# Performance work log

Measured on AMD Instinct MI355X. Metric: run time of the kernel, lower is better.

## Reference

```python
import jax, jax.numpy as jnp
import numpy as np

B, N, D, C = 8, 400, 768, 3
K = 0.4
# Original keeps ranked positions whose argsort value (original index) < k*N.
# That count is static: M = #{j in [0,N) : j < k*N}
M = int(np.sum(np.arange(N) < K * N))  # 160
# static off-diagonal pair index lists (i != j), row-major like the nested loops
_ii, _jj = np.nonzero(~np.eye(M, dtype=bool))
II = jnp.asarray(_ii)
JJ = jnp.asarray(_jj)


def setup_inputs() -> dict:
    key = jax.random.key(0)
    k1, k2, k3, k4 = jax.random.split(key, 4)
    x = jax.random.normal(k1, (B, N, D), dtype=jnp.float32)
    w_span = jax.random.normal(k2, (D, 1), dtype=jnp.float32) * 0.02
    b_span = jnp.zeros((1,), dtype=jnp.float32)
    w_pair = jax.random.normal(k3, (3 * D, C), dtype=jnp.float32) * 0.02
    b_pair = jnp.zeros((C,), dtype=jnp.float32)
    span_ranges = jax.random.randint(k4, (N, 2), 0, 40, dtype=jnp.int32)
    return {"x": x, "w_span": w_span, "b_span": b_span,
            "w_pair": w_pair, "b_pair": b_pair, "span_ranges": span_ranges}


def reference(x, w_span, b_span, w_pair, b_pair, span_ranges):
    # span scorer: Linear(D,1) + sigmoid -> [B, N]
    h = jax.nn.sigmoid(x @ w_span + b_span)[..., 0]
    # torch.argsort(descending=True)
    order = jnp.argsort(-h, axis=-1)  # [B, N], original span indices in rank order
    # keep ranked positions j where order[b, j] < k*N (exactly M per row)
    pos = jnp.sort(jnp.where(order < K * N, jnp.arange(N), N), axis=-1)[:, :M]  # [B, M]
    # gather selected spans (built under no_grad in the original)
    x_ranked = jax.lax.stop_gradient(jnp.take_along_axis(x, pos[:, :, None], axis=1))  # [B, M, D]
    ranges_ranked = span_ranges[pos]  # [B, M, 2]

    # pair scorer decomposed over the concat [x_i, x_j, x_i*x_j]
    w1, w2, w3 = w_pair[:D], w_pair[D:2 * D], w_pair[2 * D:]
    a = x_ranked @ w1  # [B, M, C] contribution of x_i
    b = x_ranked @ w2  # [B, M, C] contribution of x_j
    mult = x_ranked[:, :, None, :] * x_ranked[:, None, :, :]  # [B, M, M, D]
    logits = a[:, :, None, :] + b[:, None, :, :] + mult @ w3 + b_pair  # [B, M, M, C]
    probs = jax.nn.softmax(jax.nn.sigmoid(logits), axis=-1)

    pair_probs = probs[:, II, JJ]  # [B, M*(M-1), C], off-diagonal pairs
    pair_ranges = jnp.stack([ranges_ranked[:, II], ranges_ranked[:, JJ]], axis=2)  # [B, P, 2, 2]
    return pair_probs, pair_ranges
```

## Files before the change

### kernel.cpp

```cpp
#include <hip/hip_runtime.h>
#include <math.h>

constexpr int B_ = 8;
constexpr int N_ = 400;
constexpr int D_ = 768;
constexpr int M_ = 160;
constexpr int PAIRS_ = M_ * (M_ - 1);
constexpr size_t BMD_ = (size_t)B_ * M_ * D_;

typedef __attribute__((ext_vector_type(8))) short short8;
typedef __attribute__((ext_vector_type(4))) float floatx4;


__device__ __forceinline__ short f2bf(float f) {
  unsigned u = __float_as_uint(f);
  return (short)((u + 0x7fffu + ((u >> 16) & 1u)) >> 16);
}

__global__ __launch_bounds__(256) void k_span(const float* __restrict__ x,
                                              const float* __restrict__ w_span,
                                              double* __restrict__ z) {
  int row = blockIdx.x * 4 + (threadIdx.x >> 6);
  int lane = threadIdx.x & 63;
  const float* xr = x + (size_t)row * D_;
  double acc = 0.0;
#pragma unroll
  for (int it = 0; it < 3; ++it) {
    int d = it * 256 + lane * 4;
    float4 xv = *(const float4*)(xr + d);
    float4 wv = *(const float4*)(w_span + d);
    acc += (double)xv.x * wv.x + (double)xv.y * wv.y +
           (double)xv.z * wv.z + (double)xv.w * wv.w;
  }
#pragma unroll
  for (int off = 32; off > 0; off >>= 1)
    acc += __shfl_down(acc, off, 64);
  if (lane == 0) z[row] = acc;
}

__global__ __launch_bounds__(256) void k_rank(const double* __restrict__ z,
                                              int* __restrict__ pos) {
  __shared__ double zsh[N_];
  __shared__ int ranksh[M_];
  int b = blockIdx.x;
  int t = threadIdx.x;
  for (int j = t; j < N_; j += 256) zsh[j] = z[b * N_ + j];
  __syncthreads();
  if (t < M_) {
    double zi = zsh[t];
    int cnt = 0;
    for (int j = 0; j < N_; ++j) {
      double zj = zsh[j];
      cnt += (zj > zi) || (zj == zi && j < t);
    }
    ranksh[t] = cnt;
  }
  __syncthreads();
  if (t < M_) {
    int r = ranksh[t];
    int slot = 0;
#pragma unroll 8
    for (int k = 0; k < M_; ++k) slot += (ranksh[k] < r);
    pos[b * M_ + slot] = r;
  }
}

__global__ __launch_bounds__(256) void k_prep_ranked(const float* __restrict__ x,
                                                     const float* __restrict__ w_pair,
                                                     const float* __restrict__ b_pair,
                                                     const int* __restrict__ pos,
                                                     const int* __restrict__ span_ranges,
                                                     float* __restrict__ aterm,
                                                     float* __restrict__ bterm,
                                                     int* __restrict__ rr,
                                                     short* __restrict__ Xbf,
                                                     short* __restrict__ Ybf) {
  int s = blockIdx.x * 4 + (threadIdx.x >> 6);
  int lane = threadIdx.x & 63;
  int b = s / M_;
  int row = pos[s];
  const float* xr = x + ((size_t)(b * N_ + row)) * D_;
  const float* w3 = w_pair + 2 * D_ * 3;

  float a0 = 0, a1 = 0, a2 = 0, c0 = 0, c1 = 0, c2 = 0;
#pragma unroll
  for (int it = 0; it < 3; ++it) {
    int d = it * 256 + lane * 4;
    float4 xv = *(const float4*)(xr + d);
    float xf[4] = {xv.x, xv.y, xv.z, xv.w};

    float w1v[12], w2v[12], w3v[12];
#pragma unroll
    for (int q = 0; q < 3; ++q) {
      *(float4*)(w1v + 4 * q) = *(const float4*)(w_pair + (size_t)d * 3 + 4 * q);
      *(float4*)(w2v + 4 * q) = *(const float4*)(w_pair + (size_t)(D_ + d) * 3 + 4 * q);
      *(float4*)(w3v + 4 * q) = *(const float4*)(w3 + (size_t)d * 3 + 4 * q);
    }
#pragma unroll
    for (int e = 0; e < 4; ++e) {
      a0 += xf[e] * w1v[e * 3 + 0];
      a1 += xf[e] * w1v[e * 3 + 1];
      a2 += xf[e] * w1v[e * 3 + 2];
      c0 += xf[e] * w2v[e * 3 + 0];
      c1 += xf[e] * w2v[e * 3 + 1];
      c2 += xf[e] * w2v[e * 3 + 2];
    }

    size_t o = (size_t)s * D_ + d;
    *(short4*)(Xbf + o) = make_short4(f2bf(xf[0]), f2bf(xf[1]), f2bf(xf[2]), f2bf(xf[3]));
#pragma unroll
    for (int c = 0; c < 3; ++c) {
      *(short4*)(Ybf + (size_t)c * BMD_ + o) =
          make_short4(f2bf(xf[0] * w3v[0 * 3 + c]), f2bf(xf[1] * w3v[1 * 3 + c]),
                      f2bf(xf[2] * w3v[2 * 3 + c]), f2bf(xf[3] * w3v[3 * 3 + c]));
    }
  }
#pragma unroll
  for (int off = 32; off > 0; off >>= 1) {
    a0 += __shfl_down(a0, off, 64);
    a1 += __shfl_down(a1, off, 64);
    a2 += __shfl_down(a2, off, 64);
    c0 += __shfl_down(c0, off, 64);
    c1 += __shfl_down(c1, off, 64);
    c2 += __shfl_down(c2, off, 64);
  }
  if (lane == 0) {
    aterm[s * 3 + 0] = a0 + b_pair[0];
    aterm[s * 3 + 1] = a1 + b_pair[1];
    aterm[s * 3 + 2] = a2 + b_pair[2];
    bterm[s * 3 + 0] = c0;
    bterm[s * 3 + 1] = c1;
    bterm[s * 3 + 2] = c2;
    *(int2*)(rr + s * 2) = *(const int2*)(span_ranges + row * 2);
  }
}

__global__ __launch_bounds__(256) void k_pairs(const short* __restrict__ Xbf,
                                               const short* __restrict__ Ybf,
                                               const float* __restrict__ aterm,
                                               const float* __restrict__ bterm,
                                               const int* __restrict__ rr,
                                               float* __restrict__ out_probs,
                                               float4* __restrict__ out_ranges) {
  int lane = threadIdx.x & 63;
  int w = blockIdx.x * 4 + (threadIdx.x >> 6);
  int b = w / 100;
  int t = w - b * 100;
  int ti = t / 10;
  int tj = t - ti * 10;
  int quad = lane >> 4;
  int l16 = lane & 15;

  size_t oa = ((size_t)(b * M_ + ti * 16 + l16)) * D_ + quad * 8;
  size_t ob = ((size_t)(b * M_ + tj * 16 + l16)) * D_ + quad * 8;

  const short* ah0 = Ybf + 0 * BMD_ + oa;
  const short* ah1 = Ybf + 1 * BMD_ + oa;
  const short* ah2 = Ybf + 2 * BMD_ + oa;
  const short* bhp = Xbf + ob;

  floatx4 acc0 = {0.f, 0.f, 0.f, 0.f};
  floatx4 acc1 = {0.f, 0.f, 0.f, 0.f};
  floatx4 acc2 = {0.f, 0.f, 0.f, 0.f};

#pragma unroll 6
  for (int k = 0; k < D_; k += 32) {
    short8 bh = *(const short8*)(bhp + k);
    short8 h0 = *(const short8*)(ah0 + k);
    short8 h1 = *(const short8*)(ah1 + k);
    short8 h2 = *(const short8*)(ah2 + k);
    acc0 = __builtin_amdgcn_mfma_f32_16x16x32_bf16(h0, bh, acc0, 0, 0, 0);
    acc1 = __builtin_amdgcn_mfma_f32_16x16x32_bf16(h1, bh, acc1, 0, 0, 0);
    acc2 = __builtin_amdgcn_mfma_f32_16x16x32_bf16(h2, bh, acc2, 0, 0, 0);
  }

  const float* at = aterm + (size_t)(b * M_) * 3;
  const float* bt = bterm + (size_t)(b * M_) * 3;
  const int* rrb = rr + (size_t)(b * M_) * 2;
  int j = tj * 16 + l16;
  float bj0 = bt[j * 3 + 0], bj1 = bt[j * 3 + 1], bj2 = bt[j * 3 + 2];
  int rj0 = rrb[j * 2 + 0], rj1 = rrb[j * 2 + 1];

#pragma unroll
  for (int r = 0; r < 4; ++r) {
    int i = ti * 16 + quad * 4 + r;
    if (i == j) continue;
    float l0 = acc0[r] + at[i * 3 + 0] + bj0;
    float l1 = acc1[r] + at[i * 3 + 1] + bj1;
    float l2 = acc2[r] + at[i * 3 + 2] + bj2;
    float s0 = 1.0f / (1.0f + expf(-l0));
    float s1 = 1.0f / (1.0f + expf(-l1));
    float s2 = 1.0f / (1.0f + expf(-l2));
    float e0 = expf(s0), e1 = expf(s1), e2 = expf(s2);
    float inv = 1.0f / (e0 + e1 + e2);
    int jj = j - (j > i ? 1 : 0);
    size_t p = (size_t)b * PAIRS_ + (size_t)i * (M_ - 1) + jj;
    out_probs[p * 3 + 0] = e0 * inv;
    out_probs[p * 3 + 1] = e1 * inv;
    out_probs[p * 3 + 2] = e2 * inv;
    float4 rg;
    rg.x = (float)rrb[i * 2 + 0];
    rg.y = (float)rrb[i * 2 + 1];
    rg.z = (float)rj0;
    rg.w = (float)rj1;
    out_ranges[p] = rg;
  }
}

extern "C" void kernel_launch(void* const* d_in, const int* in_sizes, int n_in,
                              void* d_out, int out_size, void* d_ws, size_t ws_size,
                              hipStream_t stream) {
  const float* x = (const float*)d_in[0];
  const float* w_span = (const float*)d_in[1];
  const float* w_pair = (const float*)d_in[3];
  const float* b_pair = (const float*)d_in[4];
  const int* span_ranges = (const int*)d_in[5];

  char* ws = (char*)d_ws;
  double* z = (double*)ws;
  int* pos = (int*)(ws + 25600);
  float* aterm = (float*)(ws + 30720);
  float* bterm = (float*)(ws + 46080);
  int* rr = (int*)(ws + 61440);
  short* Xbf = (short*)(ws + 71680);
  short* Ybf = (short*)(ws + 2037760);

  float* out = (float*)d_out;
  float* out_probs = out;
  float4* out_ranges = (float4*)(out + (size_t)B_ * PAIRS_ * 3);

  k_span<<<(B_ * N_) / 4, 256, 0, stream>>>(x, w_span, z);
  k_rank<<<B_, 256, 0, stream>>>(z, pos);
  k_prep_ranked<<<(B_ * M_) / 4, 256, 0, stream>>>(x, w_pair, b_pair, pos,
                                                   span_ranges, aterm, bterm,
                                                   rr, Xbf, Ybf);
  k_pairs<<<(B_ * 100) / 4, 256, 0, stream>>>(Xbf, Ybf, aterm, bterm, rr,
                                              out_probs, out_ranges);
}
```

Baseline: 107.8 us.

## Exploit pair symmetry in tile MFMA and fuse ranking into prep kernel

The pair kernel now computes only upper-triangular 16x16 tiles. The x_i*x_j*w3 product is symmetric in i and j, so each off-diagonal tile writes both the (i,j) and (j,i) results, which halves the MFMA work. The ranking step is merged into the prep kernel: each block recomputes the ranks in shared memory, which removes one launch and the pos round-trip at the cost of redundant rank work in every block. BF16 conversion now uses the hardware packed convert instruction, whose rounding may differ from the manual one for NaN inputs.

```diff
diff --git a/kernel.cpp b/kernel.cpp
--- a/kernel.cpp
+++ b/kernel.cpp
@@ -7,14 +7,17 @@
 constexpr int M_ = 160;
 constexpr int PAIRS_ = M_ * (M_ - 1);
 constexpr size_t BMD_ = (size_t)B_ * M_ * D_;
+constexpr int NT_ = M_ / 16;
+constexpr int TRI_ = NT_ * (NT_ + 1) / 2;
 
 typedef __attribute__((ext_vector_type(8))) short short8;
 typedef __attribute__((ext_vector_type(4))) float floatx4;
 
 
-__device__ __forceinline__ short f2bf(float f) {
-  unsigned u = __float_as_uint(f);
-  return (short)((u + 0x7fffu + ((u >> 16) & 1u)) >> 16);
+__device__ __forceinline__ unsigned cvt_pk_bf16(float lo, float hi) {
+  unsigned r;
+  asm("v_cvt_pk_bf16_f32 %0, %1, %2" : "=v"(r) : "v"(lo), "v"(hi));
+  return r;
 }
 
 __global__ __launch_bounds__(256) void k_span(const float* __restrict__ x,
@@ -38,12 +41,23 @@
   if (lane == 0) z[row] = acc;
 }
 
-__global__ __launch_bounds__(256) void k_rank(const double* __restrict__ z,
-                                              int* __restrict__ pos) {
+__global__ __launch_bounds__(256) void k_prep_rank(const float* __restrict__ x,
+                                                   const float* __restrict__ w_pair,
+                                                   const float* __restrict__ b_pair,
+                                                   const double* __restrict__ z,
+                                                   const int* __restrict__ span_ranges,
+                                                   float* __restrict__ aterm,
+                                                   float* __restrict__ bterm,
+                                                   int* __restrict__ rr,
+                                                   short* __restrict__ Xbf,
+                                                   short* __restrict__ Ybf) {
   __shared__ double zsh[N_];
   __shared__ int ranksh[M_];
-  int b = blockIdx.x;
+  __shared__ int pos_sh[M_];
+  int blk = blockIdx.x;
+  int b = blk / 40;
   int t = threadIdx.x;
+
   for (int j = t; j < N_; j += 256) zsh[j] = z[b * N_ + j];
   __syncthreads();
   if (t < M_) {
@@ -61,24 +75,15 @@
     int slot = 0;
 #pragma unroll 8
     for (int k = 0; k < M_; ++k) slot += (ranksh[k] < r);
-    pos[b * M_ + slot] = r;
-  }
-}
-
-__global__ __launch_bounds__(256) void k_prep_ranked(const float* __restrict__ x,
-                                                     const float* __restrict__ w_pair,
-                                                     const float* __restrict__ b_pair,
-                                                     const int* __restrict__ pos,
-                                                     const int* __restrict__ span_ranges,
-                                                     float* __restrict__ aterm,
-                                                     float* __restrict__ bterm,
-                                                     int* __restrict__ rr,
-                                                     short* __restrict__ Xbf,
-                                                     short* __restrict__ Ybf) {
-  int s = blockIdx.x * 4 + (threadIdx.x >> 6);
-  int lane = threadIdx.x & 63;
-  int b = s / M_;
-  int row = pos[s];
+    pos_sh[slot] = r;
+  }
+  __syncthreads();
+
+  int wid = t >> 6;
+  int lane = t & 63;
+  int i0 = (blk % 40) * 4 + wid;
+  int s = b * M_ + i0;
+  int row = pos_sh[i0];
   const float* xr = x + ((size_t)(b * N_ + row)) * D_;
   const float* w3 = w_pair + 2 * D_ * 3;
 
@@ -107,12 +112,16 @@
     }
 
     size_t o = (size_t)s * D_ + d;
-    *(short4*)(Xbf + o) = make_short4(f2bf(xf[0]), f2bf(xf[1]), f2bf(xf[2]), f2bf(xf[3]));
+    uint2 xp;
+    xp.x = cvt_pk_bf16(xf[0], xf[1]);
+    xp.y = cvt_pk_bf16(xf[2], xf[3]);
+    *(uint2*)(Xbf + o) = xp;
 #pragma unroll
     for (int c = 0; c < 3; ++c) {
-      *(short4*)(Ybf + (size_t)c * BMD_ + o) =
-          make_short4(f2bf(xf[0] * w3v[0 * 3 + c]), f2bf(xf[1] * w3v[1 * 3 + c]),
-                      f2bf(xf[2] * w3v[2 * 3 + c]), f2bf(xf[3] * w3v[3 * 3 + c]));
+      uint2 yp;
+      yp.x = cvt_pk_bf16(xf[0] * w3v[0 * 3 + c], xf[1] * w3v[1 * 3 + c]);
+      yp.y = cvt_pk_bf16(xf[2] * w3v[2 * 3 + c], xf[3] * w3v[3 * 3 + c]);
+      *(uint2*)(Ybf + (size_t)c * BMD_ + o) = yp;
     }
   }
 #pragma unroll
@@ -144,10 +153,11 @@
                                                float4* __restrict__ out_ranges) {
   int lane = threadIdx.x & 63;
   int w = blockIdx.x * 4 + (threadIdx.x >> 6);
-  int b = w / 100;
-  int t = w - b * 100;
-  int ti = t / 10;
-  int tj = t - ti * 10;
+  int b = w / TRI_;
+  int t = w - b * TRI_;
+  int ti = 0, rem = t;
+  while (rem >= NT_ - ti) { rem -= NT_ - ti; ++ti; }
+  int tj = ti + rem;
   int quad = lane >> 4;
   int l16 = lane & 15;
 
@@ -177,33 +187,61 @@
   const float* at = aterm + (size_t)(b * M_) * 3;
   const float* bt = bterm + (size_t)(b * M_) * 3;
   const int* rrb = rr + (size_t)(b * M_) * 2;
+  bool offdiag = (ti != tj);
   int j = tj * 16 + l16;
   float bj0 = bt[j * 3 + 0], bj1 = bt[j * 3 + 1], bj2 = bt[j * 3 + 2];
+  float aj0 = at[j * 3 + 0], aj1 = at[j * 3 + 1], aj2 = at[j * 3 + 2];
   int rj0 = rrb[j * 2 + 0], rj1 = rrb[j * 2 + 1];
 
 #pragma unroll
   for (int r = 0; r < 4; ++r) {
     int i = ti * 16 + quad * 4 + r;
-    if (i == j) continue;
-    float l0 = acc0[r] + at[i * 3 + 0] + bj0;
-    float l1 = acc1[r] + at[i * 3 + 1] + bj1;
-    float l2 = acc2[r] + at[i * 3 + 2] + bj2;
-    float s0 = 1.0f / (1.0f + expf(-l0));
-    float s1 = 1.0f / (1.0f + expf(-l1));
-    float s2 = 1.0f / (1.0f + expf(-l2));
-    float e0 = expf(s0), e1 = expf(s1), e2 = expf(s2);
-    float inv = 1.0f / (e0 + e1 + e2);
-    int jj = j - (j > i ? 1 : 0);
-    size_t p = (size_t)b * PAIRS_ + (size_t)i * (M_ - 1) + jj;
-    out_probs[p * 3 + 0] = e0 * inv;
-    out_probs[p * 3 + 1] = e1 * inv;
-    out_probs[p * 3 + 2] = e2 * inv;
-    float4 rg;
-    rg.x = (float)rrb[i * 2 + 0];
-    rg.y = (float)rrb[i * 2 + 1];
-    rg.z = (float)rj0;
-    rg.w = (float)rj1;
-    out_ranges[p] = rg;
+    float ai0 = at[i * 3 + 0], ai1 = at[i * 3 + 1], ai2 = at[i * 3 + 2];
+    int ri0 = rrb[i * 2 + 0], ri1 = rrb[i * 2 + 1];
+
+    if (i != j) {
+      float l0 = acc0[r] + ai0 + bj0;
+      float l1 = acc1[r] + ai1 + bj1;
+      float l2 = acc2[r] + ai2 + bj2;
+      float s0 = 1.0f / (1.0f + expf(-l0));
+      float s1 = 1.0f / (1.0f + expf(-l1));
+      float s2 = 1.0f / (1.0f + expf(-l2));
+      float e0 = expf(s0), e1 = expf(s1), e2 = expf(s2);
+      float inv = 1.0f / (e0 + e1 + e2);
+      int jj = j - (j > i ? 1 : 0);
+      size_t p = (size_t)b * PAIRS_ + (size_t)i * (M_ - 1) + jj;
+      out_probs[p * 3 + 0] = e0 * inv;
+      out_probs[p * 3 + 1] = e1 * inv;
+      out_probs[p * 3 + 2] = e2 * inv;
+      float4 rg;
+      rg.x = (float)ri0;
+      rg.y = (float)ri1;
+      rg.z = (float)rj0;
+      rg.w = (float)rj1;
+      out_ranges[p] = rg;
+    }
+
+    if (offdiag) {
+      float bi0 = bt[i * 3 + 0], bi1 = bt[i * 3 + 1], bi2 = bt[i * 3 + 2];
+      float l0 = acc0[r] + aj0 + bi0;
+      float l1 = acc1[r] + aj1 + bi1;
+      float l2 = acc2[r] + aj2 + bi2;
+      float s0 = 1.0f / (1.0f + expf(-l0));
+      float s1 = 1.0f / (1.0f + expf(-l1));
+      float s2 = 1.0f / (1.0f + expf(-l2));
+      float e0 = expf(s0), e1 = expf(s1), e2 = expf(s2);
+      float inv = 1.0f / (e0 + e1 + e2);
+      size_t p = (size_t)b * PAIRS_ + (size_t)j * (M_ - 1) + i;
+      out_probs[p * 3 + 0] = e0 * inv;
+      out_probs[p * 3 + 1] = e1 * inv;
+      out_probs[p * 3 + 2] = e2 * inv;
+      float4 rg;
+      rg.x = (float)rj0;
+      rg.y = (float)rj1;
+      rg.z = (float)ri0;
+      rg.w = (float)ri1;
+      out_ranges[p] = rg;
+    }
   }
 }
 
@@ -218,7 +256,6 @@
 
   char* ws = (char*)d_ws;
   double* z = (double*)ws;
-  int* pos = (int*)(ws + 25600);
   float* aterm = (float*)(ws + 30720);
   float* bterm = (float*)(ws + 46080);
   int* rr = (int*)(ws + 61440);
@@ -230,10 +267,9 @@
   float4* out_ranges = (float4*)(out + (size_t)B_ * PAIRS_ * 3);
 
   k_span<<<(B_ * N_) / 4, 256, 0, stream>>>(x, w_span, z);
-  k_rank<<<B_, 256, 0, stream>>>(z, pos);
-  k_prep_ranked<<<(B_ * M_) / 4, 256, 0, stream>>>(x, w_pair, b_pair, pos,
-                                                   span_ranges, aterm, bterm,
-                                                   rr, Xbf, Ybf);
-  k_pairs<<<(B_ * 100) / 4, 256, 0, stream>>>(Xbf, Ybf, aterm, bterm, rr,
-                                              out_probs, out_ranges);
-}
+  k_prep_rank<<<(B_ * M_) / 4, 256, 0, stream>>>(x, w_pair, b_pair, z,
+                                                 span_ranges, aterm, bterm,
+                                                 rr, Xbf, Ybf);
+  k_pairs<<<(B_ * TRI_) / 4, 256, 0, stream>>>(Xbf, Ybf, aterm, bterm, rr,
+                                               out_probs, out_ranges);
+}
```

Result: no change. 108.6 us (+0.8%).
